# Optimization experiments

Hardware: AMD Instinct MI355X
Metric: run time of the kernel (lower is better)

Reference implementation:

```python
import jax, jax.numpy as jnp
import numpy as np

KE = 14.3996454784255
P = 6  # polynomial cutoff order
A_EXP = 0.3
A_PREFACTOR = 0.4543
C = jnp.array([0.1818, 0.5099, 0.2802, 0.02817], dtype=jnp.float32)
K = jnp.array([3.2, 0.9423, 0.4028, 0.2016], dtype=jnp.float32)

N_NODES = 100000
N_EDGES = 6400000
N_ELEM = 10
N_RADII = 119


def setup_inputs() -> dict:
    key = jax.random.key(0)
    k1, k2, k3, k4, k5 = jax.random.split(key, 5)
    # edge distances in a physically plausible range (avoid x ~ 0 -> 1/x blowup)
    x = jax.random.uniform(k1, (N_EDGES, 1), dtype=jnp.float32) * 4.0 + 0.05
    node_attrs = jax.random.uniform(k2, (N_NODES, N_ELEM), dtype=jnp.float32)
    edge_index = jax.random.randint(k3, (2, N_EDGES), 0, N_NODES, dtype=jnp.int64)
    atomic_numbers = jax.random.randint(k4, (N_ELEM,), 1, N_RADII, dtype=jnp.int64)
    # covalent radii table (stand-in for ase.data.covalent_radii), ~0.3..2.6 Angstrom
    covalent_radii = 0.3 + 2.3 * jax.random.uniform(k5, (N_RADII,), dtype=jnp.float32)
    return {
        "x": x,
        "node_attrs": node_attrs,
        "edge_index": edge_index,
        "atomic_numbers": atomic_numbers,
        "covalent_radii": covalent_radii,
    }


def _envelope(x, r_max, p):
    r = x / r_max
    env = (1.0
           - (p + 1.0) * (p + 2.0) / 2.0 * r ** p
           + p * (p + 2.0) * r ** (p + 1)
           - p * (p + 1.0) / 2.0 * r ** (p + 2))
    return env * (x < r_max)


def reference(x, node_attrs, edge_index, atomic_numbers, covalent_radii):
    sender = edge_index[0]    # [E]
    receiver = edge_index[1]  # [E]
    # per-node atomic number from one-hot-ish node_attrs
    node_Z = atomic_numbers[jnp.argmax(node_attrs, axis=1)][:, None]  # [N,1] int
    Z_u = node_Z[sender]   # [E,1] int
    Z_v = node_Z[receiver] # [E,1] int
    Zu_f = Z_u.astype(x.dtype)
    Zv_f = Z_v.astype(x.dtype)
    a = A_PREFACTOR * 0.529 / (Zu_f ** A_EXP + Zv_f ** A_EXP)  # [E,1]
    r_over_a = x / a
    phi = (C[0] * jnp.exp(-K[0] * r_over_a)
           + C[1] * jnp.exp(-K[1] * r_over_a)
           + C[2] * jnp.exp(-K[2] * r_over_a)
           + C[3] * jnp.exp(-K[3] * r_over_a))
    v_edges = KE * Zu_f * Zv_f / x * phi  # [E,1]
    r_max = covalent_radii[Z_u[:, 0]][:, None] + covalent_radii[Z_v[:, 0]][:, None]  # [E,1]
    env = _envelope(x, r_max, float(P))
    v_edges = 0.5 * v_edges * env
    V_ZBL = jax.ops.segment_sum(v_edges, receiver, num_segments=node_attrs.shape[0])  # [N,1]
    return V_ZBL[:, 0]
```

## Files before the change

kernel.cpp:

```cpp
#include <hip/hip_runtime.h>

#define KE_CONST 14.3996454784255f

#define P2_SHIFT 15
#define P2_CHUNK 32768
#define SCAN_B2  64
#define SCAN_THR 1024
#define MAXC     4
#define MAXE     16
#define ELEM_CAP 131072
#define DN_THR   1024
#define DN_BLOCKS 256

__global__ void zbl_prep_elem(const float* __restrict__ node_attrs,
                              unsigned char* __restrict__ elem,
                              int n_nodes, int n_elem) {
    int n = blockIdx.x * blockDim.x + threadIdx.x;
    if (n >= n_nodes) return;
    const float* row = node_attrs + (size_t)n * n_elem;
    float best = row[0];
    int bi = 0;
    for (int i = 1; i < n_elem; ++i) {
        float v = row[i];
        if (v > best) { best = v; bi = i; }
    }
    elem[n] = (unsigned char)bi;
}

__global__ void zbl_prep_pairs(const int* __restrict__ atomic_numbers,
                               const float* __restrict__ covalent_radii,
                               float4* __restrict__ pair_tab,
                               int n_elem) {
    int t = threadIdx.x;
    int np = n_elem * n_elem;
    if (t >= np) return;
    int eu = t / n_elem;
    int ev = t - eu * n_elem;
    int Zu = atomic_numbers[eu];
    int Zv = atomic_numbers[ev];
    float zu = (float)Zu, zv = (float)Zv;
    float inv_a = (__powf(zu, 0.3f) + __powf(zv, 0.3f)) * (1.0f / (0.4543f * 0.529f));
    float kezz  = 0.5f * KE_CONST * zu * zv;
    float rmax  = covalent_radii[Zu] + covalent_radii[Zv];
    pair_tab[t] = make_float4(inv_a, kezz, rmax, 1.0f / rmax);
}

__device__ __forceinline__ unsigned enc_val_p(float xv, const float4& p) {
    float t = xv * p.x;
    float phi = 0.1818f  * __expf(-3.2f    * t)
              + 0.5099f  * __expf(-0.9423f * t)
              + 0.2802f  * __expf(-0.4028f * t)
              + 0.02817f * __expf(-0.2016f * t);
    float rr = xv * p.w;
    float r2 = rr * rr;
    float r6 = r2 * r2 * r2;
    float env = 1.0f - 28.0f * r6 + 48.0f * r6 * rr - 21.0f * r6 * r2;
    float val = fmaxf(p.y * phi / xv * env, 0.0f);
    unsigned e = (__float_as_uint(val) + 0x8000u) >> 16;
    if (e > 0x7FFFu) e = 0x7FFFu;
    return (xv < p.z) ? e : 0u;
}

__global__ __launch_bounds__(DN_THR)
void zbl_dense_lds(const float* __restrict__ x,
                   const int* __restrict__ ei,
                   const unsigned char* __restrict__ elem_g,
                   const float4* __restrict__ pair_tab,
                   unsigned* __restrict__ packed,
                   int n_edges, int n_elem, int n_nodes) {
    __shared__ __align__(16) unsigned char elem[ELEM_CAP];
    __shared__ float4 pt[MAXE * MAXE];

    int np = n_elem * n_elem;
    for (int i = threadIdx.x; i < np; i += DN_THR) pt[i] = pair_tab[i];
    int nwords = (n_nodes + 15) >> 4;
    const uint4* eg4 = (const uint4*)elem_g;
    uint4* el4 = (uint4*)elem;
    for (int i = threadIdx.x; i < nwords; i += DN_THR) el4[i] = eg4[i];
    __syncthreads();

    long long e0 = (((long long)blockIdx.x * n_edges) / DN_BLOCKS) & ~3LL;
    long long e1 = (blockIdx.x == DN_BLOCKS - 1)
                     ? (long long)n_edges
                     : ((((long long)(blockIdx.x + 1) * n_edges) / DN_BLOCKS) & ~3LL);
    long long vend = e1 & ~3LL;

    for (long long b = e0 + (long long)threadIdx.x * 4; b + 4 <= vend;
         b += (long long)DN_THR * 4) {
        int4   s4 = *(const int4*)(ei + b);
        int4   r4 = *(const int4*)(ei + n_edges + b);
        float4 x4 = *(const float4*)(x + b);
        unsigned es0 = elem[s4.x], es1 = elem[s4.y], es2 = elem[s4.z], es3 = elem[s4.w];
        unsigned er0 = elem[r4.x], er1 = elem[r4.y], er2 = elem[r4.z], er3 = elem[r4.w];
        float4 p0 = pt[es0 * n_elem + er0];
        float4 p1 = pt[es1 * n_elem + er1];
        float4 p2 = pt[es2 * n_elem + er2];
        float4 p3 = pt[es3 * n_elem + er3];
        uint4 o;
        o.x = ((unsigned)r4.x << 15) | enc_val_p(x4.x, p0);
        o.y = ((unsigned)r4.y << 15) | enc_val_p(x4.y, p1);
        o.z = ((unsigned)r4.z << 15) | enc_val_p(x4.z, p2);
        o.w = ((unsigned)r4.w << 15) | enc_val_p(x4.w, p3);
        *(uint4*)(packed + b) = o;
    }
    for (long long e = vend + threadIdx.x; e < e1; e += DN_THR) {
        int r = ei[n_edges + e];
        float4 p = pt[elem[ei[e]] * n_elem + elem[r]];
        packed[e] = ((unsigned)r << 15) | enc_val_p(x[e], p);
    }
}

__global__ __launch_bounds__(SCAN_THR)
void zbl_scan(const unsigned* __restrict__ packed,
              float* __restrict__ partial,
              int n_edges) {
    unsigned c = blockIdx.x >> 6;
    int      j = blockIdx.x & (SCAN_B2 - 1);

    __shared__ __align__(16) float acc[P2_CHUNK];
    for (int i = threadIdx.x * 4; i < P2_CHUNK; i += SCAN_THR * 4)
        *(float4*)&acc[i] = make_float4(0.f, 0.f, 0.f, 0.f);
    __syncthreads();

    long long e0 = (((long long)j * n_edges) / SCAN_B2) & ~3LL;
    long long e1 = (j == SCAN_B2 - 1) ? (long long)n_edges
                                      : ((((long long)(j + 1) * n_edges) / SCAN_B2) & ~3LL);
    long long vend = e1 & ~3LL;

    for (long long b = e0 + (long long)threadIdx.x * 4; b + 4 <= vend;
         b += (long long)SCAN_THR * 4) {
        uint4 p = *(const uint4*)(packed + b);
        if ((p.x >> 30) == c) atomicAdd(&acc[(p.x >> 15) & (P2_CHUNK - 1)],
                                        __uint_as_float((p.x & 0x7FFFu) << 16));
        if ((p.y >> 30) == c) atomicAdd(&acc[(p.y >> 15) & (P2_CHUNK - 1)],
                                        __uint_as_float((p.y & 0x7FFFu) << 16));
        if ((p.z >> 30) == c) atomicAdd(&acc[(p.z >> 15) & (P2_CHUNK - 1)],
                                        __uint_as_float((p.z & 0x7FFFu) << 16));
        if ((p.w >> 30) == c) atomicAdd(&acc[(p.w >> 15) & (P2_CHUNK - 1)],
                                        __uint_as_float((p.w & 0x7FFFu) << 16));
    }
    for (long long e = vend + threadIdx.x; e < e1; e += SCAN_THR) {
        unsigned w = packed[e];
        if ((w >> 30) == c) atomicAdd(&acc[(w >> 15) & (P2_CHUNK - 1)],
                                      __uint_as_float((w & 0x7FFFu) << 16));
    }

    __syncthreads();
    float* pp = partial + (size_t)blockIdx.x * P2_CHUNK;
    for (int i = threadIdx.x * 4; i < P2_CHUNK; i += SCAN_THR * 4)
        *(float4*)(pp + i) = *(const float4*)&acc[i];
}

__global__ void zbl_reduce(const float* __restrict__ partial,
                           float* __restrict__ out,
                           int n_nodes) {
    int i = blockIdx.x * blockDim.x + threadIdx.x;
    if (i >= n_nodes) return;
    int c  = i >> P2_SHIFT;
    int li = i & (P2_CHUNK - 1);
    const float* p = partial + ((size_t)c * SCAN_B2) * P2_CHUNK + li;
    float s0 = 0.f, s1 = 0.f, s2 = 0.f, s3 = 0.f;
    #pragma unroll
    for (int j = 0; j < SCAN_B2; j += 4) {
        s0 += p[(size_t)(j + 0) * P2_CHUNK];
        s1 += p[(size_t)(j + 1) * P2_CHUNK];
        s2 += p[(size_t)(j + 2) * P2_CHUNK];
        s3 += p[(size_t)(j + 3) * P2_CHUNK];
    }
    out[i] = (s0 + s1) + (s2 + s3);
}

__global__ void zbl_node_prep(const float* __restrict__ node_attrs,
                              const int* __restrict__ atomic_numbers,
                              const float* __restrict__ covalent_radii,
                              float4* __restrict__ node_data,
                              float* __restrict__ out_zero,
                              int n_nodes, int n_elem) {
    int n = blockIdx.x * blockDim.x + threadIdx.x;
    if (n >= n_nodes) return;
    const float* row = node_attrs + (size_t)n * n_elem;
    float best = row[0];
    int bi = 0;
    for (int i = 1; i < n_elem; ++i) {
        float v = row[i];
        if (v > best) { best = v; bi = i; }
    }
    int Z = atomic_numbers[bi];
    float zf = (float)Z;
    node_data[n] = make_float4(zf, __powf(zf, 0.3f), covalent_radii[Z], 0.0f);
    out_zero[n] = 0.0f;
}

__global__ void zbl_edge_atomic(const float* __restrict__ x,
                                const int* __restrict__ edge_index,
                                const float4* __restrict__ node_data,
                                float* __restrict__ out,
                                int n_edges) {
    int e = blockIdx.x * blockDim.x + threadIdx.x;
    if (e >= n_edges) return;
    int snd = edge_index[e];
    int r = edge_index[n_edges + e];
    float xv = x[e];
    float4 du = node_data[snd];
    float4 dv = node_data[r];
    float rmax = du.z + dv.z;
    if (xv >= rmax) return;
    const float inv_a_pref = 1.0f / (0.4543f * 0.529f);
    float t = xv * (du.y + dv.y) * inv_a_pref;
    float phi = 0.1818f  * __expf(-3.2f    * t)
              + 0.5099f  * __expf(-0.9423f * t)
              + 0.2802f  * __expf(-0.4028f * t)
              + 0.02817f * __expf(-0.2016f * t);
    float v = KE_CONST * du.x * dv.x * phi / xv;
    float rr = xv / rmax;
    float r2 = rr * rr;
    float r6 = r2 * r2 * r2;
    float env = 1.0f - 28.0f * r6 + 48.0f * r6 * rr - 21.0f * r6 * r2;
    atomicAdd(&out[r], 0.5f * v * env);
}

extern "C" void kernel_launch(void* const* d_in, const int* in_sizes, int n_in,
                              void* d_out, int out_size, void* d_ws, size_t ws_size,
                              hipStream_t stream) {
    const float* x              = (const float*)d_in[0];
    const float* node_attrs     = (const float*)d_in[1];
    const int*   edge_index     = (const int*)d_in[2];
    const int*   atomic_numbers = (const int*)d_in[3];
    const float* covalent_radii = (const float*)d_in[4];
    float* out = (float*)d_out;

    int n_edges = in_sizes[0];
    int n_elem  = in_sizes[3];
    int n_nodes = in_sizes[1] / n_elem;

    int C = (n_nodes + P2_CHUNK - 1) >> P2_SHIFT;
    size_t elem_bytes   = (((size_t)n_nodes) + 255) & ~(size_t)255;
    size_t pair_bytes   = ((size_t)MAXE * MAXE * sizeof(float4) + 255) & ~(size_t)255;
    size_t packed_bytes = (((size_t)n_edges * sizeof(unsigned)) + 255) & ~(size_t)255;
    size_t part_bytes   = (size_t)C * SCAN_B2 * P2_CHUNK * sizeof(float);
    bool fast = (C >= 1) && (C <= MAXC) && (n_nodes <= ELEM_CAP) &&
                (n_elem >= 1) && (n_elem <= MAXE) &&
                (ws_size >= elem_bytes + pair_bytes + packed_bytes + part_bytes);

    if (fast) {
        unsigned char* elem     = (unsigned char*)d_ws;
        float4*        pair_tab = (float4*)((char*)d_ws + elem_bytes);
        unsigned*      packed   = (unsigned*)((char*)d_ws + elem_bytes + pair_bytes);
        float*         part     = (float*)((char*)d_ws + elem_bytes + pair_bytes + packed_bytes);

        zbl_prep_elem<<<(n_nodes + 255) / 256, 256, 0, stream>>>(
            node_attrs, elem, n_nodes, n_elem);
        zbl_prep_pairs<<<1, 256, 0, stream>>>(
            atomic_numbers, covalent_radii, pair_tab, n_elem);

        zbl_dense_lds<<<DN_BLOCKS, DN_THR, 0, stream>>>(
            x, edge_index, elem, pair_tab, packed, n_edges, n_elem, n_nodes);

        zbl_scan<<<C * SCAN_B2, SCAN_THR, 0, stream>>>(packed, part, n_edges);

        zbl_reduce<<<(n_nodes + 255) / 256, 256, 0, stream>>>(part, out, n_nodes);
        return;
    }

    float4* node_data = (float4*)d_ws;
    zbl_node_prep<<<(n_nodes + 255) / 256, 256, 0, stream>>>(
        node_attrs, atomic_numbers, covalent_radii, node_data,
        out, n_nodes, n_elem);
    zbl_edge_atomic<<<(n_edges + 255) / 256, 256, 0, stream>>>(
        x, edge_index, node_data, out, n_edges);
}
```

Baseline: 168.6 us.

## Resize scan node chunks to balance partitions and make atomics branchless

Replaces the fixed power-of-two node chunk (32768) with a chunk of 33344 nodes, so 100k nodes split into 3 chunks instead of 4, and scales blocks per chunk so the total grid stays near 256. This cuts the number of full passes over the packed edge array from 4 to 3. The per-edge membership test becomes a range check, and edges outside the chunk do an unconditional LDS atomic add of zero to a dummy slot instead of branching. Adds integer division in the reduce and extra no-op atomics, which may cause LDS contention, and the larger LDS array (about 130KB) may reduce occupancy.

```diff
diff --git a/kernel.cpp b/kernel.cpp
--- a/kernel.cpp
+++ b/kernel.cpp
@@ -2,9 +2,7 @@
 
 #define KE_CONST 14.3996454784255f
 
-#define P2_SHIFT 15
-#define P2_CHUNK 32768
-#define SCAN_B2  64
+#define CHUNK_N  33344
 #define SCAN_THR 1024
 #define MAXC     4
 #define MAXE     16
@@ -110,63 +108,68 @@
     }
 }
 
+__device__ __forceinline__ void scan_one(unsigned p, int lo, float* acc) {
+    unsigned r = p >> 15;
+    int li = (int)r - lo;
+    bool in = (unsigned)li < (unsigned)CHUNK_N;
+    float v = __uint_as_float((p & 0x7FFFu) << 16);
+    atomicAdd(&acc[in ? li : (int)(r & 8191u)], in ? v : 0.0f);
+}
+
 __global__ __launch_bounds__(SCAN_THR)
 void zbl_scan(const unsigned* __restrict__ packed,
               float* __restrict__ partial,
-              int n_edges) {
-    unsigned c = blockIdx.x >> 6;
-    int      j = blockIdx.x & (SCAN_B2 - 1);
-
-    __shared__ __align__(16) float acc[P2_CHUNK];
-    for (int i = threadIdx.x * 4; i < P2_CHUNK; i += SCAN_THR * 4)
+              int n_edges, int B2) {
+    int c = blockIdx.x / B2;
+    int j = blockIdx.x - c * B2;
+    int lo = c * CHUNK_N;
+
+    __shared__ __align__(16) float acc[CHUNK_N];
+    for (int i = threadIdx.x * 4; i < CHUNK_N; i += SCAN_THR * 4)
         *(float4*)&acc[i] = make_float4(0.f, 0.f, 0.f, 0.f);
     __syncthreads();
 
-    long long e0 = (((long long)j * n_edges) / SCAN_B2) & ~3LL;
-    long long e1 = (j == SCAN_B2 - 1) ? (long long)n_edges
-                                      : ((((long long)(j + 1) * n_edges) / SCAN_B2) & ~3LL);
+    long long e0 = (((long long)j * n_edges) / B2) & ~3LL;
+    long long e1 = (j == B2 - 1) ? (long long)n_edges
+                                 : ((((long long)(j + 1) * n_edges) / B2) & ~3LL);
     long long vend = e1 & ~3LL;
 
     for (long long b = e0 + (long long)threadIdx.x * 4; b + 4 <= vend;
          b += (long long)SCAN_THR * 4) {
         uint4 p = *(const uint4*)(packed + b);
-        if ((p.x >> 30) == c) atomicAdd(&acc[(p.x >> 15) & (P2_CHUNK - 1)],
-                                        __uint_as_float((p.x & 0x7FFFu) << 16));
-        if ((p.y >> 30) == c) atomicAdd(&acc[(p.y >> 15) & (P2_CHUNK - 1)],
-                                        __uint_as_float((p.y & 0x7FFFu) << 16));
-        if ((p.z >> 30) == c) atomicAdd(&acc[(p.z >> 15) & (P2_CHUNK - 1)],
-                                        __uint_as_float((p.z & 0x7FFFu) << 16));
-        if ((p.w >> 30) == c) atomicAdd(&acc[(p.w >> 15) & (P2_CHUNK - 1)],
-                                        __uint_as_float((p.w & 0x7FFFu) << 16));
+        scan_one(p.x, lo, acc);
+        scan_one(p.y, lo, acc);
+        scan_one(p.z, lo, acc);
+        scan_one(p.w, lo, acc);
     }
     for (long long e = vend + threadIdx.x; e < e1; e += SCAN_THR) {
         unsigned w = packed[e];
-        if ((w >> 30) == c) atomicAdd(&acc[(w >> 15) & (P2_CHUNK - 1)],
-                                      __uint_as_float((w & 0x7FFFu) << 16));
+        scan_one(w, lo, acc);
     }
 
     __syncthreads();
-    float* pp = partial + (size_t)blockIdx.x * P2_CHUNK;
-    for (int i = threadIdx.x * 4; i < P2_CHUNK; i += SCAN_THR * 4)
+    float* pp = partial + (size_t)blockIdx.x * CHUNK_N;
+    for (int i = threadIdx.x * 4; i < CHUNK_N; i += SCAN_THR * 4)
         *(float4*)(pp + i) = *(const float4*)&acc[i];
 }
 
 __global__ void zbl_reduce(const float* __restrict__ partial,
                            float* __restrict__ out,
-                           int n_nodes) {
+                           int n_nodes, int B2) {
     int i = blockIdx.x * blockDim.x + threadIdx.x;
     if (i >= n_nodes) return;
-    int c  = i >> P2_SHIFT;
-    int li = i & (P2_CHUNK - 1);
-    const float* p = partial + ((size_t)c * SCAN_B2) * P2_CHUNK + li;
+    int c  = i / CHUNK_N;
+    int li = i - c * CHUNK_N;
+    const float* p = partial + ((size_t)c * B2) * CHUNK_N + li;
     float s0 = 0.f, s1 = 0.f, s2 = 0.f, s3 = 0.f;
-    #pragma unroll
-    for (int j = 0; j < SCAN_B2; j += 4) {
-        s0 += p[(size_t)(j + 0) * P2_CHUNK];
-        s1 += p[(size_t)(j + 1) * P2_CHUNK];
-        s2 += p[(size_t)(j + 2) * P2_CHUNK];
-        s3 += p[(size_t)(j + 3) * P2_CHUNK];
-    }
+    int j = 0;
+    for (; j + 4 <= B2; j += 4) {
+        s0 += p[(size_t)(j + 0) * CHUNK_N];
+        s1 += p[(size_t)(j + 1) * CHUNK_N];
+        s2 += p[(size_t)(j + 2) * CHUNK_N];
+        s3 += p[(size_t)(j + 3) * CHUNK_N];
+    }
+    for (; j < B2; ++j) s0 += p[(size_t)j * CHUNK_N];
     out[i] = (s0 + s1) + (s2 + s3);
 }
 
@@ -233,11 +236,13 @@
     int n_elem  = in_sizes[3];
     int n_nodes = in_sizes[1] / n_elem;
 
-    int C = (n_nodes + P2_CHUNK - 1) >> P2_SHIFT;
+    int C  = (n_nodes + CHUNK_N - 1) / CHUNK_N;
+    int B2 = 256 / (C < 1 ? 1 : C);
+    if (B2 < 1) B2 = 1;
     size_t elem_bytes   = (((size_t)n_nodes) + 255) & ~(size_t)255;
     size_t pair_bytes   = ((size_t)MAXE * MAXE * sizeof(float4) + 255) & ~(size_t)255;
     size_t packed_bytes = (((size_t)n_edges * sizeof(unsigned)) + 255) & ~(size_t)255;
-    size_t part_bytes   = (size_t)C * SCAN_B2 * P2_CHUNK * sizeof(float);
+    size_t part_bytes   = (size_t)C * B2 * CHUNK_N * sizeof(float);
     bool fast = (C >= 1) && (C <= MAXC) && (n_nodes <= ELEM_CAP) &&
                 (n_elem >= 1) && (n_elem <= MAXE) &&
                 (ws_size >= elem_bytes + pair_bytes + packed_bytes + part_bytes);
@@ -256,9 +261,9 @@
         zbl_dense_lds<<<DN_BLOCKS, DN_THR, 0, stream>>>(
             x, edge_index, elem, pair_tab, packed, n_edges, n_elem, n_nodes);
 
-        zbl_scan<<<C * SCAN_B2, SCAN_THR, 0, stream>>>(packed, part, n_edges);
-
-        zbl_reduce<<<(n_nodes + 255) / 256, 256, 0, stream>>>(part, out, n_nodes);
+        zbl_scan<<<C * B2, SCAN_THR, 0, stream>>>(packed, part, n_edges, B2);
+
+        zbl_reduce<<<(n_nodes + 255) / 256, 256, 0, stream>>>(part, out, n_nodes, B2);
         return;
     }
 
```

Result: slower. 227.1 us (+34.7%).
